# Kernel tuning notes

Measured on AMD Instinct MI355X. Metric: run time of the kernel, lower is better.

Reference implementation:

```python
import jax, jax.numpy as jnp
import numpy as np

NUM_NODES = 100000
NUM_REL_P1 = 238  # num_relations + 1 (extra column for self-connection relation id -1)
B = 32768
S = 16
D_IN = 256
D_OUT = 256


def setup_inputs() -> dict:
    key = jax.random.key(0)
    k1, k2, k3, k4, k5 = jax.random.split(key, 5)
    neighbors = jax.random.randint(k1, (B, S), 0, NUM_NODES)          # sampled neighbor node ids
    relations = jax.random.randint(k2, (B, S), 0, NUM_REL_P1)          # sampled relation ids
    features = jax.random.normal(k3, (NUM_NODES, D_IN), dtype=jnp.float32)
    weight = jax.random.normal(k4, (D_OUT, D_IN), dtype=jnp.float32) * (1.0 / np.sqrt(D_IN))
    relation_weight = jax.random.normal(k5, (D_OUT, NUM_REL_P1), dtype=jnp.float32) * 0.05
    return {"neighbors": neighbors, "relations": relations, "features": features,
            "weight": weight, "relation_weight": relation_weight}


def reference(neighbors, relations, features, weight, relation_weight):
    # gather sampled neighbor embeddings: [B, S, D_in]
    neighbor_emb = features[neighbors]
    # mean-aggregate over the sample dim: [B, D_in]
    agg_neighbors = neighbor_emb.mean(axis=1)
    # linear transform: [B, D_in] @ [D_in, D_out] -> [B, D_out]
    agg_neighbors = agg_neighbors @ weight.T
    # gather + mean relation embeddings: [B, S, D_out] -> [B, D_out]
    agg_relations = relation_weight.T[relations].mean(axis=1)
    return jax.nn.relu(agg_neighbors + agg_relations)
```

## Files before the change

### kernel.cpp

```cpp
#include <hip/hip_runtime.h>

#define B_ROWS  32768
#define S_SAMP  16
#define NRELS   238
#define DIM     256
#define N_NODES 100000
#define NF4     ((N_NODES * DIM) / 4)
#define CONV_BLOCKS (NF4 / 256)

typedef __attribute__((ext_vector_type(8))) short  short8;
typedef __attribute__((ext_vector_type(8))) unsigned short ushort8;
typedef __attribute__((ext_vector_type(4))) float  f32x4;

static __device__ __forceinline__ unsigned short f2bf(float f) {
    unsigned int u = __float_as_uint(f);
    u += 0x7FFFu + ((u >> 16) & 1u);
    return (unsigned short)(u >> 16);
}
static __device__ __forceinline__ float bf2f(unsigned short u) {
    return __uint_as_float(((unsigned int)u) << 16);
}

#define GLOAD_LDS16(gp, lp)                                                      \
    __builtin_amdgcn_global_load_lds(                                            \
        (const __attribute__((address_space(1))) void*)(gp),                     \
        (__attribute__((address_space(3))) void*)(lp), 16, 0, 0)

__global__ __launch_bounds__(256) void prep_kernel(const float* __restrict__ F,
                                                   const float* __restrict__ W,
                                                   const float* __restrict__ RW,
                                                   unsigned short* __restrict__ Fb,
                                                   unsigned short* __restrict__ Wb,
                                                   unsigned short* __restrict__ RWb) {
    if (blockIdx.x < CONV_BLOCKS) {
        int i = blockIdx.x * 256 + threadIdx.x;
        float4 v = ((const float4*)F)[i];
        ushort4 p;
        p.x = f2bf(v.x); p.y = f2bf(v.y); p.z = f2bf(v.z); p.w = f2bf(v.w);
        ((ushort4*)Fb)[i] = p;
    } else {
        int i = (blockIdx.x - CONV_BLOCKS) * 256 + threadIdx.x;
        if (i < DIM * DIM) {
            Wb[i] = f2bf(W[i]);
            int n = i >> 8;
            int k = i & 255;
            RWb[i] = (k < NRELS) ? f2bf(RW[n * NRELS + k]) : (unsigned short)0;
        }
    }
}

__global__ __launch_bounds__(256, 3) void fused_kernel(const int* __restrict__ nbr,
                                                       const int* __restrict__ rels,
                                                       const unsigned short* __restrict__ Fb,
                                                       const unsigned short* __restrict__ RWb,
                                                       const unsigned short* __restrict__ Wb,
                                                       float* __restrict__ out) {
    __shared__ __align__(16) char stage[4][8192];
    __shared__ unsigned short As[32][264];
    __shared__ unsigned int   cnt4[32][32];
    unsigned short (*Cs)[264] = (unsigned short (*)[264])&stage[0][0];

    const int tid  = threadIdx.x;
    const int lane = tid & 63;
    const int wid  = __builtin_amdgcn_readfirstlane(tid >> 6);
    const int half = lane >> 5;
    const int li   = lane & 31;
    const int col0 = lane & 15;
    const int quad = lane >> 4;
    const int r0g  = blockIdx.x * 32;
    char* sbuf = &stage[wid][0];

    unsigned int* c4 = (unsigned int*)cnt4;
    c4[tid] = 0u; c4[tid + 256] = 0u; c4[tid + 512] = 0u; c4[tid + 768] = 0u;
    __syncthreads();

    {
        const int hr = tid >> 3;
        const int hs = tid & 7;
        int rid0 = rels[(r0g + hr) * S_SAMP + hs];
        int rid1 = rels[(r0g + hr) * S_SAMP + hs + 8];
        atomicAdd(&cnt4[hr][rid0 >> 3], 1u << ((rid0 & 7) * 4));
        atomicAdd(&cnt4[hr][rid1 >> 3], 1u << ((rid1 & 7) * 4));
    }

    const float sc = 1.0f / 16.0f;
    for (int i = 0; i < 8; ++i) {
        const int row_l = wid * 8 + i;
        const int2* nb2 = (const int2*)(nbr + (size_t)(r0g + row_l) * S_SAMP);
        if (i) asm volatile("s_waitcnt lgkmcnt(0)" ::: "memory");
#pragma unroll
        for (int t = 0; t < 8; ++t) {
            int2 nn = nb2[t];
            int nid = half ? nn.y : nn.x;
            GLOAD_LDS16(Fb + (size_t)nid * DIM + li * 8, sbuf + t * 1024);
        }
        asm volatile("s_waitcnt vmcnt(0)" ::: "memory");
        float af[8] = {0.f, 0.f, 0.f, 0.f, 0.f, 0.f, 0.f, 0.f};
#pragma unroll
        for (int t = 0; t < 8; ++t) {
            ushort8 f = *(const ushort8*)(sbuf + (2 * t + half) * 512 + li * 16);
#pragma unroll
            for (int j = 0; j < 8; ++j) af[j] += bf2f(f[j]);
        }
        ushort8 pk;
#pragma unroll
        for (int j = 0; j < 8; ++j) {
            float full = af[j] + __shfl_xor(af[j], 32, 64);
            pk[j] = f2bf(full * sc);
        }
        if (!half) *(ushort8*)&As[row_l][li * 8] = pk;
    }

    short8 Breg[4][4];
#pragma unroll
    for (int j = 0; j < 4; ++j)
#pragma unroll
        for (int kk = 0; kk < 4; ++kk)
            Breg[j][kk] = *(const short8*)(Wb + (size_t)((wid * 4 + j) * 16 + col0) * DIM
                                              + kk * 32 + quad * 8);
    __syncthreads();

    {
        const int rr = tid >> 3;
        const int kb = (tid & 7) * 32;
#pragma unroll
        for (int g = 0; g < 4; ++g) {
            unsigned int w = cnt4[rr][(kb >> 3) + g];
            ushort8 ck;
#pragma unroll
            for (int j = 0; j < 8; ++j)
                ck[j] = f2bf((float)((w >> (4 * j)) & 0xFu) * 0.0625f);
            *(ushort8*)&Cs[rr][kb + g * 8] = ck;
        }
    }
    __syncthreads();

    f32x4 acc[2][4];
#pragma unroll
    for (int mt = 0; mt < 2; ++mt)
#pragma unroll
        for (int j = 0; j < 4; ++j) acc[mt][j] = (f32x4){0.f, 0.f, 0.f, 0.f};

#pragma unroll
    for (int mt = 0; mt < 2; ++mt) {
        const int mrow = mt * 16 + col0;
#pragma unroll
        for (int kk = 0; kk < 4; ++kk) {
            short8 a = *(const short8*)&As[mrow][kk * 32 + quad * 8];
#pragma unroll
            for (int j = 0; j < 4; ++j)
                acc[mt][j] = __builtin_amdgcn_mfma_f32_16x16x32_bf16(a, Breg[j][kk], acc[mt][j], 0, 0, 0);
        }
    }
#pragma unroll
    for (int j = 0; j < 4; ++j)
#pragma unroll
        for (int kk = 0; kk < 4; ++kk)
            Breg[j][kk] = *(const short8*)(Wb + (size_t)((wid * 4 + j) * 16 + col0) * DIM
                                              + (kk + 4) * 32 + quad * 8);
#pragma unroll
    for (int mt = 0; mt < 2; ++mt) {
        const int mrow = mt * 16 + col0;
#pragma unroll
        for (int kk = 0; kk < 4; ++kk) {
            short8 a = *(const short8*)&As[mrow][(kk + 4) * 32 + quad * 8];
#pragma unroll
            for (int j = 0; j < 4; ++j)
                acc[mt][j] = __builtin_amdgcn_mfma_f32_16x16x32_bf16(a, Breg[j][kk], acc[mt][j], 0, 0, 0);
        }
    }
#pragma unroll
    for (int j = 0; j < 4; ++j)
#pragma unroll
        for (int kk = 0; kk < 4; ++kk)
            Breg[j][kk] = *(const short8*)(RWb + (size_t)((wid * 4 + j) * 16 + col0) * DIM
                                               + kk * 32 + quad * 8);
#pragma unroll
    for (int mt = 0; mt < 2; ++mt) {
        const int mrow = mt * 16 + col0;
#pragma unroll
        for (int kk = 0; kk < 4; ++kk) {
            short8 a = *(const short8*)&Cs[mrow][kk * 32 + quad * 8];
#pragma unroll
            for (int j = 0; j < 4; ++j)
                acc[mt][j] = __builtin_amdgcn_mfma_f32_16x16x32_bf16(a, Breg[j][kk], acc[mt][j], 0, 0, 0);
        }
    }
#pragma unroll
    for (int j = 0; j < 4; ++j)
#pragma unroll
        for (int kk = 0; kk < 4; ++kk)
            Breg[j][kk] = *(const short8*)(RWb + (size_t)((wid * 4 + j) * 16 + col0) * DIM
                                               + (kk + 4) * 32 + quad * 8);
#pragma unroll
    for (int mt = 0; mt < 2; ++mt) {
        const int mrow = mt * 16 + col0;
#pragma unroll
        for (int kk = 0; kk < 4; ++kk) {
            short8 a = *(const short8*)&Cs[mrow][(kk + 4) * 32 + quad * 8];
#pragma unroll
            for (int j = 0; j < 4; ++j)
                acc[mt][j] = __builtin_amdgcn_mfma_f32_16x16x32_bf16(a, Breg[j][kk], acc[mt][j], 0, 0, 0);
        }
    }

#pragma unroll
    for (int mt = 0; mt < 2; ++mt) {
#pragma unroll
        for (int j = 0; j < 4; ++j) {
            const int col = (wid * 4 + j) * 16 + col0;
#pragma unroll
            for (int i2 = 0; i2 < 4; ++i2) {
                const int r_l = mt * 16 + quad * 4 + i2;
                float v = acc[mt][j][i2];
                out[(size_t)(r0g + r_l) * DIM + col] = v > 0.f ? v : 0.f;
            }
        }
    }
}

extern "C" void kernel_launch(void* const* d_in, const int* in_sizes, int n_in,
                              void* d_out, int out_size, void* d_ws, size_t ws_size,
                              hipStream_t stream) {
    const int*   neighbors = (const int*)d_in[0];
    const int*   relations = (const int*)d_in[1];
    const float* features  = (const float*)d_in[2];
    const float* weight    = (const float*)d_in[3];
    const float* relw      = (const float*)d_in[4];
    float* out = (float*)d_out;

    char* ws = (char*)d_ws;
    unsigned short* Wb  = (unsigned short*)ws;
    unsigned short* RWb = (unsigned short*)(ws + 131072);
    unsigned short* Fb  = (unsigned short*)(ws + 262144);

    prep_kernel<<<CONV_BLOCKS + 256, 256, 0, stream>>>(features, weight, relw, Fb, Wb, RWb);
    fused_kernel<<<B_ROWS / 32, 256, 0, stream>>>(neighbors, relations, Fb, RWb, Wb, out);
}
```

Before: 232.2 us.

## Software-pipeline neighbor gathers with triple-buffered LDS chunks

```diff
diff --git a/kernel.cpp b/kernel.cpp
--- a/kernel.cpp
+++ b/kernel.cpp
@@ -55,7 +55,7 @@
                                                        const unsigned short* __restrict__ RWb,
                                                        const unsigned short* __restrict__ Wb,
                                                        float* __restrict__ out) {
-    __shared__ __align__(16) char stage[4][8192];
+    __shared__ __align__(16) char stage[4][6144];
     __shared__ unsigned short As[32][264];
     __shared__ unsigned int   cnt4[32][32];
     unsigned short (*Cs)[264] = (unsigned short (*)[264])&stage[0][0];
@@ -83,33 +83,53 @@
         atomicAdd(&cnt4[hr][rid1 >> 3], 1u << ((rid1 & 7) * 4));
     }
 
+    const int2 my = ((const int2*)(nbr + (size_t)(r0g + wid * 8) * S_SAMP))[lane];
     const float sc = 1.0f / 16.0f;
-    for (int i = 0; i < 8; ++i) {
-        const int row_l = wid * 8 + i;
-        const int2* nb2 = (const int2*)(nbr + (size_t)(r0g + row_l) * S_SAMP);
-        if (i) asm volatile("s_waitcnt lgkmcnt(0)" ::: "memory");
-#pragma unroll
-        for (int t = 0; t < 8; ++t) {
-            int2 nn = nb2[t];
-            int nid = half ? nn.y : nn.x;
-            GLOAD_LDS16(Fb + (size_t)nid * DIM + li * 8, sbuf + t * 1024);
-        }
-        asm volatile("s_waitcnt vmcnt(0)" ::: "memory");
-        float af[8] = {0.f, 0.f, 0.f, 0.f, 0.f, 0.f, 0.f, 0.f};
-#pragma unroll
-        for (int t = 0; t < 8; ++t) {
-            ushort8 f = *(const ushort8*)(sbuf + (2 * t + half) * 512 + li * 16);
-#pragma unroll
-            for (int j = 0; j < 8; ++j) af[j] += bf2f(f[j]);
-        }
-        ushort8 pk;
-#pragma unroll
-        for (int j = 0; j < 8; ++j) {
-            float full = af[j] + __shfl_xor(af[j], 32, 64);
-            pk[j] = f2bf(full * sc);
-        }
-        if (!half) *(ushort8*)&As[row_l][li * 8] = pk;
-    }
+    float af[8];
+
+#define ISSUE_CHUNK(k)                                                            \
+    {                                                                             \
+        const int i_ = (k) >> 2, q_ = (k) & 3;                                    \
+        const int h_ = i_ * 8 + 2 * q_;                                           \
+        int ax0 = __shfl(my.x, h_),     ay0 = __shfl(my.y, h_);                   \
+        int ax1 = __shfl(my.x, h_ + 1), ay1 = __shfl(my.y, h_ + 1);               \
+        int n0 = half ? ay0 : ax0;                                                \
+        int n1 = half ? ay1 : ax1;                                                \
+        asm volatile("s_waitcnt lgkmcnt(0)" ::: "memory");                        \
+        GLOAD_LDS16(Fb + (size_t)n0 * DIM + li * 8, sbuf + ((k) % 3) * 2048);     \
+        GLOAD_LDS16(Fb + (size_t)n1 * DIM + li * 8, sbuf + ((k) % 3) * 2048 + 1024);\
+    }
+
+    ISSUE_CHUNK(0);
+    ISSUE_CHUNK(1);
+#pragma unroll
+    for (int k = 0; k < 32; ++k) {
+        if (k < 31) asm volatile("s_waitcnt vmcnt(2)" ::: "memory");
+        else        asm volatile("s_waitcnt vmcnt(0)" ::: "memory");
+        if (k + 2 < 32) ISSUE_CHUNK(k + 2);
+        if ((k & 3) == 0) {
+#pragma unroll
+            for (int j = 0; j < 8; ++j) af[j] = 0.f;
+        }
+        {
+            const char* cb = sbuf + (k % 3) * 2048 + half * 512 + li * 16;
+            ushort8 f0 = *(const ushort8*)(cb);
+            ushort8 f1 = *(const ushort8*)(cb + 1024);
+#pragma unroll
+            for (int j = 0; j < 8; ++j) af[j] += bf2f(f0[j]) + bf2f(f1[j]);
+        }
+        if ((k & 3) == 3) {
+            const int row_l = wid * 8 + (k >> 2);
+            ushort8 pk;
+#pragma unroll
+            for (int j = 0; j < 8; ++j) {
+                float full = af[j] + __shfl_xor(af[j], 32, 64);
+                pk[j] = f2bf(full * sc);
+            }
+            if (!half) *(ushort8*)&As[row_l][li * 8] = pk;
+        }
+    }
+#undef ISSUE_CHUNK
 
     short8 Breg[4][4];
 #pragma unroll
```

After: 233.6 us. No clear change (+0.6%).
